# Optimization experiments

Hardware: AMD Instinct MI355X
Metric: run time of the kernel (lower is better)

Reference implementation:

```python
import jax, jax.numpy as jnp
import numpy as np

# Dimensions: N sites, B batch, D bond dim, d physical dim, C output classes
N, B, D, d, C = 1024, 256, 16, 2, 10
STDDEV = 1e-5
INIT_DIAG = 1.0


def setup_inputs() -> dict:
    key = jax.random.key(0)
    k1, k2, k3 = jax.random.split(key, 3)
    x = jax.random.normal(k1, (N, B, d), dtype=jnp.float32)
    eye = jnp.eye(D, dtype=jnp.float32)
    # tensor[n,:,:,i] = init_diag * I + stddev * noise  (matches TF init)
    tensor = INIT_DIAG * eye[None, :, :, None] + STDDEV * jax.random.normal(k2, (N, D, D, d), dtype=jnp.float32)
    # Aout[c] = I + stddev * noise
    Aout = eye[None, :, :] + STDDEV * jax.random.normal(k3, (C, D, D), dtype=jnp.float32)
    return {"x": x, "tensor": tensor, "Aout": Aout}


def _chain_prod(A):
    # A: (n, b, D, D) -> ordered matrix-chain product (b, D, D), log-depth tree.
    # Faithful to parallel_contract: pairwise einsum per level; odd leftover is
    # kept at the end of the list (order-preserving, associativity-equivalent).
    while A.shape[0] > 1:
        n = A.shape[0]
        half = n // 2
        prod = jnp.einsum('nblk,nbkr->nblr', A[0:2 * half:2], A[1:2 * half:2])
        if n % 2 == 1:
            prod = jnp.concatenate([prod, A[-1:]], axis=0)
        A = prod
    return A[0]


def reference(x, tensor, Aout):
    # A: (N, B, D, D) site matrices after contracting input features
    A = jnp.einsum('nbi,nlri->nblr', x, tensor)
    nhalf = A.shape[0] // 2
    # Left half product, take row 0 (left boundary); right half, take col 0
    Al = _chain_prod(A[:nhalf])[:, 0, :]   # (B, D)
    Ar = _chain_prod(A[nhalf:])[:, :, 0]   # (B, D)
    # out[b,o] = Al[b] @ Aout[o] @ Ar[b]
    return jnp.einsum('bl,olr,br->bo', Al, Aout, Ar)
```

## Files before the change

kernel.cpp:

```cpp
#include <hip/hip_runtime.h>


#define BATCH  256
#define NCLS   10
#define NSITES 1024
#define NGRP   16
#define SEGLEN 16
#define NB     8

typedef __attribute__((ext_vector_type(4))) float f32x4;
typedef __attribute__((ext_vector_type(2))) float f32x2;
typedef __attribute__((ext_vector_type(4))) short short4b;
typedef __attribute__((ext_vector_type(2))) unsigned uint2v;
typedef __attribute__((ext_vector_type(4))) unsigned uint4v;
typedef __attribute__((ext_vector_type(4))) unsigned short us4;
typedef __attribute__((ext_vector_type(8))) short short8;

static __device__ __forceinline__ unsigned short bf16tr(float f) {
    return (unsigned short)(__builtin_bit_cast(unsigned, f) >> 16);
}
static __device__ __forceinline__ unsigned short bf16rne(float f) {
    unsigned u = __builtin_bit_cast(unsigned, f);
    u += 0x7FFFu + ((u >> 16) & 1u);
    return (unsigned short)(u >> 16);
}
static __device__ __forceinline__ float bf16tof(unsigned short h) {
    return __builtin_bit_cast(float, (unsigned)h << 16);
}
static __device__ __forceinline__ unsigned fbits(float f) {
    return __builtin_bit_cast(unsigned, f);
}
static __device__ __forceinline__ float lo16(unsigned u) {
    return __builtin_bit_cast(float, u << 16);
}
static __device__ __forceinline__ float hi16(unsigned u) {
    return __builtin_bit_cast(float, u & 0xffff0000u);
}
static __device__ __forceinline__ unsigned pkhi(float hi, float lo) {
    return __builtin_amdgcn_perm(fbits(hi), fbits(lo), 0x07060302u);
}
static __device__ __forceinline__ short4b mk4(unsigned lo, unsigned hi) {
    uint2v u; u.x = lo; u.y = hi;
    return __builtin_bit_cast(short4b, u);
}
static __device__ __forceinline__ f32x2 pfma(f32x2 a, f32x2 b, f32x2 c) {
#if __has_builtin(__builtin_elementwise_fma)
    return __builtin_elementwise_fma(a, b, c);
#else
    return a * b + c;
#endif
}
static __device__ __forceinline__ f32x4 mfma16(short4b a, short4b b, f32x4 c) {
#if __has_builtin(__builtin_amdgcn_mfma_f32_16x16x16bf16_1k)
    return __builtin_amdgcn_mfma_f32_16x16x16bf16_1k(a, b, c, 0, 0, 0);
#else
    f32x4 d;
    asm volatile("v_mfma_f32_16x16x16_bf16 %0, %1, %2, %3"
                 : "=v"(d) : "v"(a), "v"(b), "v"(c));
    return d;
#endif
}

__global__ __launch_bounds__(256) void ta_pack_kernel(
    const float* __restrict__ tensor, unsigned short* __restrict__ Ta)
{
    __shared__ float s[512];
    const int n = blockIdx.x, t = threadIdx.x;
    *(float2*)(s + 2 * t) = *(const float2*)(tensor + (size_t)n * 512 + 2 * t);
    __syncthreads();
    const int o0 = 2 * t;
    const int lane = o0 >> 3, e0 = o0 & 7;
    const int q = lane >> 4, m = lane & 15;
    const int i = e0 >> 2, j0 = e0 & 3;
    const int k0 = 4 * q + j0;
    const float v0 = s[k0 * 32 + m * 2 + i];
    const float v1 = s[(k0 + 1) * 32 + m * 2 + i];
    ((unsigned*)Ta)[(size_t)n * 256 + t] =
        (unsigned)bf16rne(v0) | ((unsigned)bf16rne(v1) << 16);
}

__global__ __launch_bounds__(256) void chain_kernel(
    const float* __restrict__ x,
    const unsigned short* __restrict__ Ta,
    unsigned short* __restrict__ M2)
{
    __shared__ __align__(16) unsigned short rm[32 * 256];
    __shared__ __align__(16) unsigned short cm[32 * 256];
    const int t = threadIdx.x, wave = t >> 6, lane = t & 63;
    const int quad = lane >> 4, l15 = lane & 15;
    const int bt = blockIdx.x & 31, g = blockIdx.x >> 5;
    const int b0 = bt * NB;
    const int seg = g * 4 + wave, n0 = seg * SEGLEN;

    f32x4 d[NB];
#pragma unroll
    for (int j = 0; j < NB; ++j)
#pragma unroll
        for (int r = 0; r < 4; ++r) d[j][r] = (quad * 4 + r == l15) ? 1.0f : 0.0f;

    const uint4v* __restrict__ tp = (const uint4v*)Ta + (size_t)n0 * 64 + lane;

#pragma unroll 4
    for (int s = 0; s < SEGLEN; ++s) {
        const int n = n0 + s;
        const uint4v tw = tp[(size_t)s * 64];
        const float4* __restrict__ xp =
            (const float4*)(x + ((size_t)n * BATCH + b0) * 2);
        const float4 xq0 = xp[0], xq1 = xp[1], xq2 = xp[2], xq3 = xp[3];
        const float xs0[NB] = {xq0.x, xq0.z, xq1.x, xq1.z, xq2.x, xq2.z, xq3.x, xq3.z};
        const float xs1[NB] = {xq0.y, xq0.w, xq1.y, xq1.w, xq2.y, xq2.w, xq3.y, xq3.w};
        const f32x2 ta01 = {lo16(tw.x), hi16(tw.x)};
        const f32x2 ta23 = {lo16(tw.y), hi16(tw.y)};
        const f32x2 tb01 = {lo16(tw.z), hi16(tw.z)};
        const f32x2 tb23 = {lo16(tw.w), hi16(tw.w)};
#pragma unroll
        for (int j = 0; j < NB; ++j) {
            const f32x2 xa = {xs0[j], xs0[j]};
            const f32x2 xb = {xs1[j], xs1[j]};
            const f32x2 a01 = pfma(xa, ta01, xb * tb01);
            const f32x2 a23 = pfma(xa, ta23, xb * tb23);
            const short4b af = mk4(pkhi(a01[1], a01[0]), pkhi(a23[1], a23[0]));
            const short4b wb = mk4(pkhi(d[j][1], d[j][0]), pkhi(d[j][3], d[j][2]));
            f32x4 c0 = {0.0f, 0.0f, 0.0f, 0.0f};
            d[j] = mfma16(af, wb, c0);
        }
    }

    if (wave & 1) {
#pragma unroll
        for (int j = 0; j < NB; ++j) {
            const int sl = j * 4 + wave;
#pragma unroll
            for (int r = 0; r < 4; ++r)
                rm[sl * 256 + (quad * 4 + r) * 16 + l15] = bf16tr(d[j][r]);
        }
    } else {
#pragma unroll
        for (int j = 0; j < NB; ++j) {
            const int sl = j * 4 + wave;
            us4 pk = {bf16tr(d[j][0]), bf16tr(d[j][1]), bf16tr(d[j][2]), bf16tr(d[j][3])};
            *(us4*)(cm + sl * 256 + l15 * 16 + quad * 4) = pk;
        }
    }
    __syncthreads();

    short4b af1v[4], bf1v[4];
#pragma unroll
    for (int i = 0; i < 4; ++i) {
        const int p = 4 * wave + i, j = p >> 1, h = p & 1;
        af1v[i] = __builtin_bit_cast(short4b,
            *(const uint2v*)(rm + (j * 4 + 2 * h + 1) * 256 + l15 * 16 + quad * 4));
        bf1v[i] = __builtin_bit_cast(short4b,
            *(const uint2v*)(cm + (j * 4 + 2 * h) * 256 + l15 * 16 + quad * 4));
    }
    __syncthreads();
#pragma unroll
    for (int i = 0; i < 4; ++i) {
        const int p = 4 * wave + i, j = p >> 1, h = p & 1;
        f32x4 c0 = {0.0f, 0.0f, 0.0f, 0.0f};
        f32x4 q = mfma16(af1v[i], bf1v[i], c0);
        const int sl = j * 4 + h;
        if (h) {
#pragma unroll
            for (int r = 0; r < 4; ++r)
                rm[sl * 256 + (quad * 4 + r) * 16 + l15] = bf16tr(q[r]);
        } else {
            us4 pk = {bf16tr(q[0]), bf16tr(q[1]), bf16tr(q[2]), bf16tr(q[3])};
            *(us4*)(cm + sl * 256 + l15 * 16 + quad * 4) = pk;
        }
    }
    __syncthreads();

#pragma unroll
    for (int i = 0; i < 2; ++i) {
        const int j = 2 * wave + i;
        const short4b af2 = __builtin_bit_cast(short4b,
            *(const uint2v*)(rm + (j * 4 + 1) * 256 + l15 * 16 + quad * 4));
        const short4b bf2 = __builtin_bit_cast(short4b,
            *(const uint2v*)(cm + (j * 4 + 0) * 256 + l15 * 16 + quad * 4));
        f32x4 c0 = {0.0f, 0.0f, 0.0f, 0.0f};
        f32x4 rr = mfma16(af2, bf2, c0);
        us4 pk = {bf16tr(rr[0]), bf16tr(rr[1]), bf16tr(rr[2]), bf16tr(rr[3])};
        *(us4*)(M2 + ((size_t)(b0 + j) * NGRP + g) * 256 + l15 * 16 + quad * 4) = pk;
    }
}

__global__ __launch_bounds__(256) void combine_kernel(
    const unsigned short* __restrict__ M2,
    const float* __restrict__ Aout,
    float* __restrict__ out)
{
    __shared__ __align__(16) unsigned short rm[16 * 256];
    __shared__ __align__(16) unsigned short cm[16 * 256];
    const int b = blockIdx.x, t = threadIdx.x;
    const int wave = t >> 6, lane = t & 63, quad = lane >> 4, l15 = lane & 15;

    const short8* __restrict__ src = (const short8*)(M2 + (size_t)b * NGRP * 256);
#pragma unroll
    for (int i2 = 0; i2 < 2; ++i2) {
        const int i = t + 256 * i2;
        const short8 v = src[i];
        *((short8*)cm + i) = v;
        const int mat = i >> 5, c = (i >> 1) & 15, r0 = (i & 1) * 8;
#pragma unroll
        for (int e = 0; e < 8; ++e)
            rm[mat * 256 + (r0 + e) * 16 + c] = (unsigned short)v[e];
    }
    __syncthreads();

    for (int lvl = 0; lvl < 3; ++lvl) {
        const int np = 8 >> lvl;
        short4b afr[2], bfr[2];
        int pids[2], nmine = 0;
        for (int p = wave; p < np; p += 4) {
            afr[nmine] = __builtin_bit_cast(short4b,
                 *(const uint2v*)(rm + (2 * p + 1) * 256 + l15 * 16 + quad * 4));
            bfr[nmine] = __builtin_bit_cast(short4b,
                 *(const uint2v*)(cm + (2 * p) * 256 + l15 * 16 + quad * 4));
            pids[nmine] = p; ++nmine;
        }
        __syncthreads();
        for (int ii = 0; ii < nmine; ++ii) {
            f32x4 c0 = {0.0f, 0.0f, 0.0f, 0.0f};
            f32x4 r = mfma16(afr[ii], bfr[ii], c0);
            const int p = pids[ii];
#pragma unroll
            for (int rr = 0; rr < 4; ++rr)
                rm[p * 256 + (quad * 4 + rr) * 16 + l15] = bf16tr(r[rr]);
            us4 pk = {bf16tr(r[0]), bf16tr(r[1]), bf16tr(r[2]), bf16tr(r[3])};
            *(us4*)(cm + p * 256 + l15 * 16 + quad * 4) = pk;
        }
        __syncthreads();
    }

    if (t < NCLS * 16) {
        const int o = t >> 4, r = t & 15;
        const float vr = bf16tof(rm[256 + r]);
        float s = 0.0f;
#pragma unroll
        for (int l = 0; l < 16; ++l)
            s = __builtin_fmaf(bf16tof(rm[l * 16]), Aout[((size_t)o * 16 + l) * 16 + r], s);
        s *= vr;
#pragma unroll
        for (int off = 8; off > 0; off >>= 1)
            s += __shfl_xor(s, off, 16);
        if (r == 0) out[(size_t)b * NCLS + o] = s;
    }
}

extern "C" void kernel_launch(void* const* d_in, const int* in_sizes, int n_in,
                              void* d_out, int out_size, void* d_ws, size_t ws_size,
                              hipStream_t stream)
{
    const float* x      = (const float*)d_in[0];
    const float* tensor = (const float*)d_in[1];
    const float* Aout   = (const float*)d_in[2];
    float* out = (float*)d_out;

    unsigned short* Ta = (unsigned short*)d_ws;
    unsigned short* M2 = (unsigned short*)((char*)d_ws + (1 << 20));

    ta_pack_kernel<<<NSITES, 256, 0, stream>>>(tensor, Ta);
    chain_kernel<<<BATCH * NGRP / NB, 256, 0, stream>>>(x, Ta, M2);
    combine_kernel<<<BATCH, 256, 0, stream>>>(M2, Aout, out);
}
```

Measured before the change: 76.18 us.

## Fuse tensor bf16 packing into chain kernel with 512-thread blocks

Removes the separate ta_pack_kernel launch and instead has each chain block load its 64 sites of fp32 tensor data, pack them to bf16 into shared memory, and reuse them across 16 batch elements split over 8 waves. Blocks double to 512 threads and NB doubles to 16, so each block covers twice the batch and the grid halves. One launch and the global round trip of the packed tensor go away, at the cost of redundant packing per batch tile, a larger shared buffer (64KB) and truncation instead of round-to-nearest for the tensor values.

Result: slower. 77.71 us (+2.0%).

```diff
diff --git a/kernel.cpp b/kernel.cpp
--- a/kernel.cpp
+++ b/kernel.cpp
@@ -6,7 +6,7 @@
 #define NSITES 1024
 #define NGRP   16
 #define SEGLEN 16
-#define NB     8
+#define NB     16
 
 typedef __attribute__((ext_vector_type(4))) float f32x4;
 typedef __attribute__((ext_vector_type(2))) float f32x2;
@@ -18,11 +18,6 @@
 
 static __device__ __forceinline__ unsigned short bf16tr(float f) {
     return (unsigned short)(__builtin_bit_cast(unsigned, f) >> 16);
-}
-static __device__ __forceinline__ unsigned short bf16rne(float f) {
-    unsigned u = __builtin_bit_cast(unsigned, f);
-    u += 0x7FFFu + ((u >> 16) & 1u);
-    return (unsigned short)(u >> 16);
 }
 static __device__ __forceinline__ float bf16tof(unsigned short h) {
     return __builtin_bit_cast(float, (unsigned)h << 16);
@@ -61,62 +56,62 @@
 #endif
 }
 
-__global__ __launch_bounds__(256) void ta_pack_kernel(
-    const float* __restrict__ tensor, unsigned short* __restrict__ Ta)
-{
-    __shared__ float s[512];
-    const int n = blockIdx.x, t = threadIdx.x;
-    *(float2*)(s + 2 * t) = *(const float2*)(tensor + (size_t)n * 512 + 2 * t);
-    __syncthreads();
-    const int o0 = 2 * t;
-    const int lane = o0 >> 3, e0 = o0 & 7;
-    const int q = lane >> 4, m = lane & 15;
-    const int i = e0 >> 2, j0 = e0 & 3;
-    const int k0 = 4 * q + j0;
-    const float v0 = s[k0 * 32 + m * 2 + i];
-    const float v1 = s[(k0 + 1) * 32 + m * 2 + i];
-    ((unsigned*)Ta)[(size_t)n * 256 + t] =
-        (unsigned)bf16rne(v0) | ((unsigned)bf16rne(v1) << 16);
-}
-
-__global__ __launch_bounds__(256) void chain_kernel(
+__global__ __launch_bounds__(512) void chain_kernel(
     const float* __restrict__ x,
-    const unsigned short* __restrict__ Ta,
+    const float* __restrict__ tensor,
     unsigned short* __restrict__ M2)
 {
-    __shared__ __align__(16) unsigned short rm[32 * 256];
-    __shared__ __align__(16) unsigned short cm[32 * 256];
-    const int t = threadIdx.x, wave = t >> 6, lane = t & 63;
+    __shared__ __align__(16) unsigned short buf[32768];
+    const int t = threadIdx.x, w = t >> 6, lane = t & 63;
     const int quad = lane >> 4, l15 = lane & 15;
-    const int bt = blockIdx.x & 31, g = blockIdx.x >> 5;
+    const int bt = blockIdx.x & 15, g = blockIdx.x >> 4;
     const int b0 = bt * NB;
-    const int seg = g * 4 + wave, n0 = seg * SEGLEN;
-
-    f32x4 d[NB];
-#pragma unroll
-    for (int j = 0; j < NB; ++j)
+
+#pragma unroll
+    for (int s8 = 0; s8 < 8; ++s8) {
+        const int site = s8 * 8 + w;
+        const int n = g * 64 + site;
+        const float* __restrict__ ts =
+            tensor + (size_t)n * 512 + ((size_t)(4 * quad) * 16 + l15) * 2;
+        const float2 v0 = *(const float2*)(ts);
+        const float2 v1 = *(const float2*)(ts + 32);
+        const float2 v2 = *(const float2*)(ts + 64);
+        const float2 v3 = *(const float2*)(ts + 96);
+        uint4v pk;
+        pk.x = pkhi(v1.x, v0.x);
+        pk.y = pkhi(v3.x, v2.x);
+        pk.z = pkhi(v1.y, v0.y);
+        pk.w = pkhi(v3.y, v2.y);
+        *(uint4v*)(buf + site * 512 + lane * 8) = pk;
+    }
+    __syncthreads();
+
+    const int sw = w & 3, hb = w >> 2;
+    const int n0loc = sw * 16, n0 = g * 64 + n0loc;
+    const int bb = b0 + hb * 8;
+
+    f32x4 d[8];
+#pragma unroll
+    for (int j = 0; j < 8; ++j)
 #pragma unroll
         for (int r = 0; r < 4; ++r) d[j][r] = (quad * 4 + r == l15) ? 1.0f : 0.0f;
-
-    const uint4v* __restrict__ tp = (const uint4v*)Ta + (size_t)n0 * 64 + lane;
 
 #pragma unroll 4
     for (int s = 0; s < SEGLEN; ++s) {
-        const int n = n0 + s;
-        const uint4v tw = tp[(size_t)s * 64];
-        const float4* __restrict__ xp =
-            (const float4*)(x + ((size_t)n * BATCH + b0) * 2);
-        const float4 xq0 = xp[0], xq1 = xp[1], xq2 = xp[2], xq3 = xp[3];
-        const float xs0[NB] = {xq0.x, xq0.z, xq1.x, xq1.z, xq2.x, xq2.z, xq3.x, xq3.z};
-        const float xs1[NB] = {xq0.y, xq0.w, xq1.y, xq1.w, xq2.y, xq2.w, xq3.y, xq3.w};
+        const uint4v tw = *(const uint4v*)(buf + (n0loc + s) * 512 + lane * 8);
+        const float2* __restrict__ xp =
+            (const float2*)(x + ((size_t)(n0 + s) * BATCH + bb) * 2);
+        float2 xj[8];
+#pragma unroll
+        for (int j = 0; j < 8; ++j) xj[j] = xp[j];
         const f32x2 ta01 = {lo16(tw.x), hi16(tw.x)};
         const f32x2 ta23 = {lo16(tw.y), hi16(tw.y)};
         const f32x2 tb01 = {lo16(tw.z), hi16(tw.z)};
         const f32x2 tb23 = {lo16(tw.w), hi16(tw.w)};
 #pragma unroll
-        for (int j = 0; j < NB; ++j) {
-            const f32x2 xa = {xs0[j], xs0[j]};
-            const f32x2 xb = {xs1[j], xs1[j]};
+        for (int j = 0; j < 8; ++j) {
+            const f32x2 xa = {xj[j].x, xj[j].x};
+            const f32x2 xb = {xj[j].y, xj[j].y};
             const f32x2 a01 = pfma(xa, ta01, xb * tb01);
             const f32x2 a23 = pfma(xa, ta23, xb * tb23);
             const short4b af = mk4(pkhi(a01[1], a01[0]), pkhi(a23[1], a23[0]));
@@ -126,20 +121,22 @@
         }
     }
 
-    if (wave & 1) {
-#pragma unroll
-        for (int j = 0; j < NB; ++j) {
-            const int sl = j * 4 + wave;
+    __syncthreads();
+
+    if (sw & 1) {
+#pragma unroll
+        for (int j = 0; j < 8; ++j) {
+            const int sl = (hb * 8 + j) * 4 + sw;
 #pragma unroll
             for (int r = 0; r < 4; ++r)
-                rm[sl * 256 + (quad * 4 + r) * 16 + l15] = bf16tr(d[j][r]);
+                buf[sl * 256 + (quad * 4 + r) * 16 + l15] = bf16tr(d[j][r]);
         }
     } else {
 #pragma unroll
-        for (int j = 0; j < NB; ++j) {
-            const int sl = j * 4 + wave;
+        for (int j = 0; j < 8; ++j) {
+            const int sl = (hb * 8 + j) * 4 + sw;
             us4 pk = {bf16tr(d[j][0]), bf16tr(d[j][1]), bf16tr(d[j][2]), bf16tr(d[j][3])};
-            *(us4*)(cm + sl * 256 + l15 * 16 + quad * 4) = pk;
+            *(us4*)(buf + sl * 256 + l15 * 16 + quad * 4) = pk;
         }
     }
     __syncthreads();
@@ -147,41 +144,41 @@
     short4b af1v[4], bf1v[4];
 #pragma unroll
     for (int i = 0; i < 4; ++i) {
-        const int p = 4 * wave + i, j = p >> 1, h = p & 1;
+        const int p = 4 * w + i, jb = p >> 1, h = p & 1;
         af1v[i] = __builtin_bit_cast(short4b,
-            *(const uint2v*)(rm + (j * 4 + 2 * h + 1) * 256 + l15 * 16 + quad * 4));
+            *(const uint2v*)(buf + (jb * 4 + 2 * h + 1) * 256 + l15 * 16 + quad * 4));
         bf1v[i] = __builtin_bit_cast(short4b,
-            *(const uint2v*)(cm + (j * 4 + 2 * h) * 256 + l15 * 16 + quad * 4));
+            *(const uint2v*)(buf + (jb * 4 + 2 * h) * 256 + l15 * 16 + quad * 4));
     }
     __syncthreads();
 #pragma unroll
     for (int i = 0; i < 4; ++i) {
-        const int p = 4 * wave + i, j = p >> 1, h = p & 1;
+        const int p = 4 * w + i, jb = p >> 1, h = p & 1;
         f32x4 c0 = {0.0f, 0.0f, 0.0f, 0.0f};
         f32x4 q = mfma16(af1v[i], bf1v[i], c0);
-        const int sl = j * 4 + h;
+        const int sl = jb * 4 + h;
         if (h) {
 #pragma unroll
             for (int r = 0; r < 4; ++r)
-                rm[sl * 256 + (quad * 4 + r) * 16 + l15] = bf16tr(q[r]);
+                buf[sl * 256 + (quad * 4 + r) * 16 + l15] = bf16tr(q[r]);
         } else {
             us4 pk = {bf16tr(q[0]), bf16tr(q[1]), bf16tr(q[2]), bf16tr(q[3])};
-            *(us4*)(cm + sl * 256 + l15 * 16 + quad * 4) = pk;
+            *(us4*)(buf + sl * 256 + l15 * 16 + quad * 4) = pk;
         }
     }
     __syncthreads();
 
 #pragma unroll
     for (int i = 0; i < 2; ++i) {
-        const int j = 2 * wave + i;
+        const int jb = 2 * w + i;
         const short4b af2 = __builtin_bit_cast(short4b,
-            *(const uint2v*)(rm + (j * 4 + 1) * 256 + l15 * 16 + quad * 4));
+            *(const uint2v*)(buf + (jb * 4 + 1) * 256 + l15 * 16 + quad * 4));
         const short4b bf2 = __builtin_bit_cast(short4b,
-            *(const uint2v*)(cm + (j * 4 + 0) * 256 + l15 * 16 + quad * 4));
+            *(const uint2v*)(buf + (jb * 4 + 0) * 256 + l15 * 16 + quad * 4));
         f32x4 c0 = {0.0f, 0.0f, 0.0f, 0.0f};
         f32x4 rr = mfma16(af2, bf2, c0);
         us4 pk = {bf16tr(rr[0]), bf16tr(rr[1]), bf16tr(rr[2]), bf16tr(rr[3])};
-        *(us4*)(M2 + ((size_t)(b0 + j) * NGRP + g) * 256 + l15 * 16 + quad * 4) = pk;
+        *(us4*)(M2 + ((size_t)(b0 + jb) * NGRP + g) * 256 + l15 * 16 + quad * 4) = pk;
     }
 }
 
@@ -257,10 +254,8 @@
     const float* Aout   = (const float*)d_in[2];
     float* out = (float*)d_out;
 
-    unsigned short* Ta = (unsigned short*)d_ws;
-    unsigned short* M2 = (unsigned short*)((char*)d_ws + (1 << 20));
-
-    ta_pack_kernel<<<NSITES, 256, 0, stream>>>(tensor, Ta);
-    chain_kernel<<<BATCH * NGRP / NB, 256, 0, stream>>>(x, Ta, M2);
+    unsigned short* M2 = (unsigned short*)d_ws;
+
+    chain_kernel<<<BATCH * NGRP / NB, 512, 0, stream>>>(x, tensor, M2);
     combine_kernel<<<BATCH, 256, 0, stream>>>(M2, Aout, out);
 }
```
